# Performance work log

Measured on AMD Instinct MI355X. Metric: run time of the kernel, lower is better.

Reference implementation:

```python
import jax, jax.numpy as jnp
import numpy as np

B, T, K, H = 8, 1024, 512, 8
MASKED = True

def setup_inputs() -> dict:
    key = jax.random.key(0)
    ks = jax.random.split(key, 6)
    s = 0.02
    return {
        "x": jax.random.normal(ks[0], (B, T, K), dtype=jnp.float32),
        "Wq": jax.random.normal(ks[1], (K, H * K), dtype=jnp.float32) * s,
        "Wk": jax.random.normal(ks[2], (K, H * K), dtype=jnp.float32) * s,
        "Wv": jax.random.normal(ks[3], (K, H * K), dtype=jnp.float32) * s,
        "Wu": jax.random.normal(ks[4], (H * K, K), dtype=jnp.float32) * s,
        "bu": jnp.zeros((K,), dtype=jnp.float32),
    }

def reference(x, Wq, Wk, Wv, Wu, bu):
    b, t, k = x.shape
    h = H
    scale = k ** (-0.25)  # applied to both q and k, as in the torch module
    q = (x @ Wq).reshape(b, t, h, k) * scale
    kk = (x @ Wk).reshape(b, t, h, k) * scale
    v = (x @ Wv).reshape(b, t, h, k)
    # scores: [b, h, t_q, t_k]
    dot = jnp.einsum("bthk,bshk->bhts", q, kk)
    if MASKED:
        causal = jnp.tril(jnp.ones((t, t), dtype=bool))
        dot = jnp.where(causal, dot, -jnp.inf)
    attn = jax.nn.softmax(dot, axis=-1)
    out = jnp.einsum("bhts,bshk->bthk", attn, v).reshape(b, t, h * k)
    return out @ Wu + bu
```

## Files before the change

kernel.cpp:

```cpp
#include <hip/hip_runtime.h>
#include <hip/hip_bf16.h>

#define T_SEQ 1024
#define NH 8
#define DH 512
#define HK 4096

typedef __attribute__((ext_vector_type(8))) __bf16 bf16x8;
typedef __attribute__((ext_vector_type(4))) float f32x4;

#define QK_SCALE 0.21022410381342863f
#define QK_SCALE_LOG2E 0.30328926584f

static __device__ __forceinline__ unsigned short f2bu(float f) {
  union { __hip_bfloat16 h; unsigned short u; } cv;
  cv.h = __float2bfloat16(f);
  return cv.u;
}

#define GLOAD_LDS16(gsrc, ldst) \
  __builtin_amdgcn_global_load_lds((const __attribute__((address_space(1))) void*)(gsrc), \
                                   (__attribute__((address_space(3))) void*)(ldst), 16, 0, 0)

__global__ void cvt_bf16_kernel(const float* __restrict__ in, unsigned short* __restrict__ out, int n4) {
  int i = blockIdx.x * blockDim.x + threadIdx.x;
  if (i >= n4) return;
  const float4 v = reinterpret_cast<const float4*>(in)[i];
  ushort4 u; u.x = f2bu(v.x); u.y = f2bu(v.y); u.z = f2bu(v.z); u.w = f2bu(v.w);
  reinterpret_cast<ushort4*>(out)[i] = u;
}

__global__ void transpose_cvt_kernel(const float* __restrict__ in, unsigned short* __restrict__ out,
                                     int R, int C) {
  __shared__ float tile[32][33];
  const int c0 = blockIdx.x * 32, r0 = blockIdx.y * 32;
  const int tx = threadIdx.x, ty = threadIdx.y;
  #pragma unroll
  for (int i = ty; i < 32; i += 8)
    tile[i][tx] = in[(size_t)(r0 + i) * C + (c0 + tx)];
  __syncthreads();
  #pragma unroll
  for (int i = ty; i < 32; i += 8)
    out[(size_t)(c0 + i) * R + (r0 + tx)] = f2bu(tile[tx][i]);
}

__global__ void transpose_cvt3_kernel(const float* __restrict__ Wq, const float* __restrict__ Wk,
                                      const float* __restrict__ Wv, unsigned short* __restrict__ out) {
  __shared__ float tile[32][33];
  const float* in = (blockIdx.z == 0) ? Wq : (blockIdx.z == 1) ? Wk : Wv;
  unsigned short* dst = out + (size_t)blockIdx.z * 4096 * 512;
  const int c0 = blockIdx.x * 32, r0 = blockIdx.y * 32;
  const int tx = threadIdx.x, ty = threadIdx.y;
  #pragma unroll
  for (int i = ty; i < 32; i += 8)
    tile[i][tx] = in[(size_t)(r0 + i) * 4096 + (c0 + tx)];
  __syncthreads();
  #pragma unroll
  for (int i = ty; i < 32; i += 8)
    dst[(size_t)(c0 + i) * 512 + (r0 + tx)] = f2bu(tile[tx][i]);
}

__global__ __launch_bounds__(512, 1)
void gemm_qkv(const unsigned short* __restrict__ A,
              const unsigned short* __restrict__ B,
              unsigned short* __restrict__ Qo,
              unsigned short* __restrict__ Ko,
              unsigned short* __restrict__ Vo) {
  __shared__ __align__(16) char smem[131072];
  const int tid = threadIdx.x, lane = tid & 63, w = tid >> 6;
  const int wm = w >> 2, wn = w & 3;
  const int bid = blockIdx.x;
  const int x = bid & 7, inner = bid >> 3;
  const int p0 = (x * 6 + inner % 6) * 256;
  const int p1 = (inner / 6) * 256;

  f32x4 acc[8][4];
  #pragma unroll
  for (int i = 0; i < 8; ++i)
    #pragma unroll
    for (int j = 0; j < 4; ++j)
      acc[i][j] = f32x4{0.f, 0.f, 0.f, 0.f};

  auto stage = [&](int t, int c) {
    const int kt = t * 128;
    #pragma unroll
    for (int is = 0; is < 4; ++is) {
      const int ob = is * 8192 + w * 1024;
      const int ol = ob + lane * 16;
      const int row = ol >> 7, bo = ol & 127;
      const int sw = (row & 7) << 4;
      GLOAD_LDS16((const char*)A + (size_t)(p0 + row) * 1024 + kt + (bo ^ sw),
                  smem + c * 32768 + ob);
      GLOAD_LDS16((const char*)B + (size_t)(p1 + row) * 1024 + kt + (bo ^ sw),
                  smem + 65536 + c * 32768 + ob);
    }
  };

  stage(0, 0);
  stage(1, 1);
  asm volatile("s_waitcnt vmcnt(8)" ::: "memory");
  __builtin_amdgcn_sched_barrier(0);
  __builtin_amdgcn_s_barrier();

  for (int t = 0; t < 8; ++t) {
    const int c = t & 1;
    const char* Ab = smem + c * 32768;
    const char* Bb = smem + 65536 + c * 32768;
    #pragma unroll
    for (int ks = 0; ks < 2; ++ks) {
      bf16x8 af[8], bf[4];
      #pragma unroll
      for (int mi = 0; mi < 8; ++mi) {
        const int row = wm * 128 + mi * 16 + (lane & 15);
        af[mi] = *reinterpret_cast<const bf16x8*>(
            Ab + row * 128 + ((ks * 64 + ((lane >> 4) << 4)) ^ ((row & 7) << 4)));
      }
      #pragma unroll
      for (int ni = 0; ni < 4; ++ni) {
        const int row = wn * 64 + ni * 16 + (lane & 15);
        bf[ni] = *reinterpret_cast<const bf16x8*>(
            Bb + row * 128 + ((ks * 64 + ((lane >> 4) << 4)) ^ ((row & 7) << 4)));
      }
      #pragma unroll
      for (int mi = 0; mi < 8; ++mi)
        #pragma unroll
        for (int ni = 0; ni < 4; ++ni)
          acc[mi][ni] = __builtin_amdgcn_mfma_f32_16x16x32_bf16(af[mi], bf[ni], acc[mi][ni], 0, 0, 0);
    }
    asm volatile("" ::: "memory");
    __builtin_amdgcn_sched_barrier(0);
    __builtin_amdgcn_s_barrier();
    if (t + 2 < 8) stage(t + 2, c);
    if (t + 1 < 8) {
      if (t + 2 < 8) asm volatile("s_waitcnt vmcnt(8)" ::: "memory");
      else           asm volatile("s_waitcnt vmcnt(0)" ::: "memory");
      __builtin_amdgcn_sched_barrier(0);
      __builtin_amdgcn_s_barrier();
    }
  }

  const int region = p0 >> 12;
  if (region < 2) {
    const float qs = (region == 0) ? QK_SCALE_LOG2E : QK_SCALE;
    unsigned short* dst = (region == 0) ? Qo : Ko;
    #pragma unroll
    for (int mi = 0; mi < 8; ++mi) {
      #pragma unroll
      for (int ni = 0; ni < 4; ++ni) {
        const int n = p0 + wm * 128 + mi * 16 + ((lane >> 4) << 2);
        const int m = p1 + wn * 64 + ni * 16 + (lane & 15);
        const int b = m >> 10, t = m & 1023;
        const int nr = n & 4095, h = nr >> 9, d = nr & 511;
        ushort4 u;
        u.x = f2bu(acc[mi][ni][0] * qs); u.y = f2bu(acc[mi][ni][1] * qs);
        u.z = f2bu(acc[mi][ni][2] * qs); u.w = f2bu(acc[mi][ni][3] * qs);
        *reinterpret_cast<ushort4*>(&dst[((size_t)((b * NH + h) * T_SEQ + t)) * DH + d]) = u;
      }
    }
  } else {
    __builtin_amdgcn_sched_barrier(0);
    __builtin_amdgcn_s_barrier();
    unsigned short* Vl = reinterpret_cast<unsigned short*>(smem);
    #pragma unroll
    for (int mi = 0; mi < 8; ++mi) {
      #pragma unroll
      for (int ni = 0; ni < 4; ++ni) {
        const int dl0 = wm * 128 + mi * 16 + ((lane >> 4) << 2);
        const int tl = wn * 64 + ni * 16 + (lane & 15);
        #pragma unroll
        for (int r = 0; r < 4; ++r) {
          const int dl = dl0 + r;
          Vl[dl * 256 + (tl ^ ((dl & 7) << 3))] = f2bu(acc[mi][ni][r]);
        }
      }
    }
    __syncthreads();
    const int bb = p1 >> 10, t0 = p1 & 1023;
    const int hh = (p0 - 8192) >> 9, d0 = (p0 - 8192) & 511;
    unsigned short* vdst = Vo + ((size_t)(bb * NH + hh) * DH + d0) * T_SEQ + t0;
    #pragma unroll
    for (int i = 0; i < 16; ++i) {
      const int idx = i * 512 + tid;
      const int dr = idx >> 5, tc = (idx & 31) * 8;
      *reinterpret_cast<uint4*>(vdst + (size_t)dr * T_SEQ + tc) =
          *reinterpret_cast<const uint4*>(Vl + dr * 256 + (tc ^ ((dr & 7) << 3)));
    }
  }
}

__global__ __launch_bounds__(256, 4)
void gemm_out(const unsigned short* __restrict__ A,
              const unsigned short* __restrict__ B,
              const float* __restrict__ bias,
              float* __restrict__ C) {
  __shared__ __align__(16) char As[8192];
  __shared__ __align__(16) char Bs[16384];
  const int tid = threadIdx.x, lane = tid & 63, w = tid >> 6;
  const int bid = blockIdx.x;
  const int x = bid & 7, inner = bid >> 3;
  const int mtiles_per_xcd = gridDim.x >> 7;
  const int c0 = (inner & 15) * 32;
  const int m0 = (x * mtiles_per_xcd + (inner >> 4)) * 64;
  const int Kd = HK;

  f32x4 acc[2];
  acc[0] = f32x4{0.f, 0.f, 0.f, 0.f};
  acc[1] = f32x4{0.f, 0.f, 0.f, 0.f};

  for (int kt = 0; kt < Kd; kt += 128) {
    __syncthreads();
    #pragma unroll
    for (int is = 0; is < 2; ++is) {
      const int ob = is * 4096 + w * 1024;
      const int ol = ob + lane * 16;
      const int row = ol >> 8, bo = ol & 255;
      GLOAD_LDS16((const char*)A + ((size_t)(c0 + row) * Kd + kt) * 2 + (bo ^ ((row & 15) << 4)), As + ob);
    }
    #pragma unroll
    for (int is = 0; is < 4; ++is) {
      const int ob = is * 4096 + w * 1024;
      const int ol = ob + lane * 16;
      const int row = ol >> 8, bo = ol & 255;
      GLOAD_LDS16((const char*)B + ((size_t)(m0 + row) * Kd + kt) * 2 + (bo ^ ((row & 15) << 4)), Bs + ob);
    }
    __syncthreads();
    #pragma unroll
    for (int ks = 0; ks < 4; ++ks) {
      const int ko = ks * 64 + ((lane >> 4) << 4);
      bf16x8 af0, af1, bf;
      { const int row = (lane & 15);
        af0 = *reinterpret_cast<const bf16x8*>(As + row * 256 + (ko ^ ((row & 15) << 4))); }
      { const int row = 16 + (lane & 15);
        af1 = *reinterpret_cast<const bf16x8*>(As + row * 256 + (ko ^ ((row & 15) << 4))); }
      { const int row = w * 16 + (lane & 15);
        bf = *reinterpret_cast<const bf16x8*>(Bs + row * 256 + (ko ^ ((row & 15) << 4))); }
      acc[0] = __builtin_amdgcn_mfma_f32_16x16x32_bf16(af0, bf, acc[0], 0, 0, 0);
      acc[1] = __builtin_amdgcn_mfma_f32_16x16x32_bf16(af1, bf, acc[1], 0, 0, 0);
    }
  }

  const int m = m0 + w * 16 + (lane & 15);
  #pragma unroll
  for (int fc = 0; fc < 2; ++fc) {
    const int c = c0 + fc * 16 + ((lane >> 4) << 2);
    const float4 bn = *reinterpret_cast<const float4*>(&bias[c]);
    float4 v;
    v.x = acc[fc][0] + bn.x; v.y = acc[fc][1] + bn.y;
    v.z = acc[fc][2] + bn.z; v.w = acc[fc][3] + bn.w;
    *reinterpret_cast<float4*>(&C[(size_t)m * DH + c]) = v;
  }
}

__global__ __launch_bounds__(512, 1)
void attn_kernel(const unsigned short* __restrict__ Qg,
                 const unsigned short* __restrict__ Kg,
                 const unsigned short* __restrict__ Vtg,
                 unsigned short* __restrict__ Og) {
  __shared__ __align__(16) char Ks[2][32768];
  __shared__ __align__(16) char Vts[2][32768];
  __shared__ float S_lds[64 * 32];
  __shared__ __align__(16) char P_lds[64 * 64];
  __shared__ float Mrow[64], Lrow[64], Arow[64];
  __shared__ int rflag;

  const int tid = threadIdx.x, lane = tid & 63, w = tid >> 6;
  const int n = blockIdx.x;
  const int h = n & 7, p = (n >> 3) & 7, b = n >> 6;
  const int bh = b * NH + h;

  const unsigned short* Qbase = Qg + (size_t)bh * T_SEQ * DH;
  const char* Kbase = (const char*)(Kg + (size_t)bh * T_SEQ * DH);
  const char* Vbase = (const char*)(Vtg + (size_t)bh * DH * T_SEQ);

  auto stage = [&](int st, int buf) {
    #pragma unroll
    for (int is = 0; is < 4; ++is) {
      const int ob = is * 8192 + w * 1024;
      const int ol = ob + lane * 16;
      { const int row = ol >> 10, bo = ol & 1023;
        GLOAD_LDS16(Kbase + (size_t)(st * 32 + row) * 1024 + (bo ^ ((row & 7) << 4)), Ks[buf] + ob); }
      { const int row = ol >> 6, bo = ol & 63;
        GLOAD_LDS16(Vbase + (size_t)row * 2048 + st * 64 + (bo ^ ((row & 3) << 4)), Vts[buf] + ob); }
    }
  };

  for (int rep = 0; rep < 2; ++rep) {
    const int qt = rep ? 15 - p : p;
    const int nst = 2 * qt + 2;
    __syncthreads();

    bf16x8 qreg[16];
    {
      const int qrow = qt * 64 + ((w >> 1) << 4) + (lane & 15);
      const unsigned short* qp = Qbase + (size_t)qrow * DH + ((lane >> 4) << 3);
      #pragma unroll
      for (int k2 = 0; k2 < 16; ++k2)
        qreg[k2] = *reinterpret_cast<const bf16x8*>(qp + k2 * 32);
    }

    f32x4 o[2][8];
    #pragma unroll
    for (int mi = 0; mi < 2; ++mi)
      #pragma unroll
      for (int ni = 0; ni < 8; ++ni)
        o[mi][ni] = f32x4{0.f, 0.f, 0.f, 0.f};

    if (tid < 64) { Mrow[tid] = -INFINITY; Lrow[tid] = 0.f; }

    int cur = 0;
    stage(0, 0);

    for (int st = 0; st < nst; ++st) {
      __syncthreads();
      if (st + 1 < nst) stage(st + 1, cur ^ 1);
      if (tid == 0) rflag = 0;

      {
        const int krow = ((w & 1) << 4) + (lane & 15);
        const char* kr = Ks[cur] + krow * 1024;
        const int sw = (krow & 7) << 4;
        f32x4 sA = f32x4{0.f, 0.f, 0.f, 0.f};
        f32x4 sB = f32x4{0.f, 0.f, 0.f, 0.f};
        __builtin_amdgcn_s_setprio(1);
        #pragma unroll
        for (int ks = 0; ks < 16; ks += 2) {
          bf16x8 kf0 = *reinterpret_cast<const bf16x8*>(kr + ((ks * 64 + ((lane >> 4) << 4)) ^ sw));
          bf16x8 kf1 = *reinterpret_cast<const bf16x8*>(kr + (((ks + 1) * 64 + ((lane >> 4) << 4)) ^ sw));
          sA = __builtin_amdgcn_mfma_f32_16x16x32_bf16(qreg[ks], kf0, sA, 0, 0, 0);
          sB = __builtin_amdgcn_mfma_f32_16x16x32_bf16(qreg[ks + 1], kf1, sB, 0, 0, 0);
        }
        __builtin_amdgcn_s_setprio(0);
        const f32x4 s = sA + sB;
        const int col = ((w & 1) << 4) + (lane & 15);
        const int rbase = ((w >> 1) << 4) + ((lane >> 4) << 2);
        #pragma unroll
        for (int r = 0; r < 4; ++r)
          S_lds[(rbase + r) * 32 + (col ^ (((rbase + r) & 7) << 2))] = s[r];
      }
      asm volatile("s_waitcnt lgkmcnt(0)" ::: "memory");
      __builtin_amdgcn_sched_barrier(0);
      __builtin_amdgcn_s_barrier();

      {
        const int r = tid >> 3, cg = tid & 7;
        const int grow = qt * 64 + r;
        const int base = r * 32 + ((cg * 4) ^ ((r & 7) << 2));
        float sv[4];
        #pragma unroll
        for (int j = 0; j < 4; ++j) {
          const int c = cg * 4 + j;
          const float x = S_lds[base + j];
          sv[j] = (st * 32 + c > grow) ? -INFINITY : x;
        }
        float pm = fmaxf(fmaxf(sv[0], sv[1]), fmaxf(sv[2], sv[3]));
        pm = fmaxf(pm, __shfl_xor(pm, 1));
        pm = fmaxf(pm, __shfl_xor(pm, 2));
        pm = fmaxf(pm, __shfl_xor(pm, 4));
        const float m_old = Mrow[r];
        const bool defer = (pm <= m_old + 11.0f);
        const float m_new = defer ? m_old : pm;
        float ps;
        ushort4 pu;
        { float p0 = exp2f(sv[0] - m_new), p1 = exp2f(sv[1] - m_new),
                p2 = exp2f(sv[2] - m_new), p3 = exp2f(sv[3] - m_new);
          ps = p0 + p1 + p2 + p3;
          pu.x = f2bu(p0); pu.y = f2bu(p1); pu.z = f2bu(p2); pu.w = f2bu(p3); }
        *reinterpret_cast<ushort4*>(P_lds + r * 64 + ((cg * 8) ^ ((r & 3) << 4))) = pu;
        ps += __shfl_xor(ps, 1);
        ps += __shfl_xor(ps, 2);
        ps += __shfl_xor(ps, 4);
        if (cg == 0) {
          const float alpha = defer ? 1.0f : exp2f(m_old - m_new);
          if (!defer) { rflag = 1; Mrow[r] = m_new; }
          Arow[r] = alpha;
          Lrow[r] = alpha * Lrow[r] + ps;
        }
      }
      asm volatile("s_waitcnt lgkmcnt(0)" ::: "memory");
      __builtin_amdgcn_sched_barrier(0);
      __builtin_amdgcn_s_barrier();

      {
        bf16x8 pf[2];
        #pragma unroll
        for (int mi = 0; mi < 2; ++mi) {
          const int pr = ((w >> 2) << 5) + mi * 16 + (lane & 15);
          pf[mi] = *reinterpret_cast<const bf16x8*>(
              P_lds + pr * 64 + ((((lane >> 4) << 4)) ^ ((pr & 3) << 4)));
        }
        if (rflag) {
          #pragma unroll
          for (int mi = 0; mi < 2; ++mi) {
            const int rb = ((w >> 2) << 5) + mi * 16 + ((lane >> 4) << 2);
            const f32x4 al = f32x4{Arow[rb], Arow[rb + 1], Arow[rb + 2], Arow[rb + 3]};
            #pragma unroll
            for (int ni = 0; ni < 8; ++ni) o[mi][ni] *= al;
          }
        }
        __builtin_amdgcn_s_setprio(1);
        #pragma unroll
        for (int ni = 0; ni < 8; ++ni) {
          const int vr = ((w & 3) << 7) + ni * 16 + (lane & 15);
          bf16x8 vf = *reinterpret_cast<const bf16x8*>(
              Vts[cur] + vr * 64 + ((((lane >> 4) << 4)) ^ ((vr & 3) << 4)));
          o[0][ni] = __builtin_amdgcn_mfma_f32_16x16x32_bf16(pf[0], vf, o[0][ni], 0, 0, 0);
          o[1][ni] = __builtin_amdgcn_mfma_f32_16x16x32_bf16(pf[1], vf, o[1][ni], 0, 0, 0);
        }
        __builtin_amdgcn_s_setprio(0);
      }
      cur ^= 1;
    }

    #pragma unroll
    for (int mi = 0; mi < 2; ++mi) {
      const int rb = ((w >> 2) << 5) + mi * 16 + ((lane >> 4) << 2);
      f32x4 li;
      #pragma unroll
      for (int r = 0; r < 4; ++r) li[r] = 1.f / Lrow[rb + r];
      #pragma unroll
      for (int ni = 0; ni < 8; ++ni) {
        const int d = ((w & 3) << 7) + ni * 16 + (lane & 15);
        const size_t base = ((size_t)(b * T_SEQ + qt * 64 + rb) * NH + h) * DH + d;
        #pragma unroll
        for (int r = 0; r < 4; ++r)
          Og[base + (size_t)r * NH * DH] = f2bu(o[mi][ni][r] * li[r]);
      }
    }
  }
}

extern "C" void kernel_launch(void* const* d_in, const int* in_sizes, int n_in,
                              void* d_out, int out_size, void* d_ws, size_t ws_size,
                              hipStream_t stream) {
  (void)in_sizes; (void)n_in; (void)out_size;
  const float* x  = (const float*)d_in[0];
  const float* Wq = (const float*)d_in[1];
  const float* Wk = (const float*)d_in[2];
  const float* Wv = (const float*)d_in[3];
  const float* Wu = (const float*)d_in[4];
  const float* bu = (const float*)d_in[5];
  float* out = (float*)d_out;

  const size_t PERS = (size_t)8192 * 512 * 2 + 3 * (size_t)4096 * 512 * 2 + (size_t)512 * 4096 * 2;
  int NB = 8;
  while (NB > 1 && PERS + 4 * ((size_t)NB * 1024 * 4096 * 2) + 65536 > ws_size) NB >>= 1;

  size_t off = 0;
  auto wsp = [&](size_t bytes) {
    char* p = (char*)d_ws + off;
    off += (bytes + 255) & ~(size_t)255;
    return p;
  };
  unsigned short* xb   = (unsigned short*)wsp((size_t)8192 * 512 * 2);
  unsigned short* Wcat = (unsigned short*)wsp(3 * (size_t)4096 * 512 * 2);
  unsigned short* Wut  = (unsigned short*)wsp((size_t)512 * 4096 * 2);
  const size_t CHB = (size_t)NB * 1024 * 4096 * 2;
  unsigned short* Qc = (unsigned short*)wsp(CHB);
  unsigned short* Kc = (unsigned short*)wsp(CHB);
  unsigned short* Vc = (unsigned short*)wsp(CHB);
  unsigned short* Oc = (unsigned short*)wsp(CHB);

  cvt_bf16_kernel<<<4096, 256, 0, stream>>>(x, xb, 8192 * 512 / 4);
  transpose_cvt3_kernel<<<dim3(128, 16, 3), dim3(32, 8), 0, stream>>>(Wq, Wk, Wv, Wcat);
  transpose_cvt_kernel<<<dim3(16, 128), dim3(32, 8), 0, stream>>>(Wu, Wut, 4096, 512);

  const int nchunks = 8 / NB;
  for (int c = 0; c < nchunks; ++c) {
    const unsigned short* xc = xb + (size_t)c * NB * 1024 * 512;
    gemm_qkv<<<192 * NB, 512, 0, stream>>>(Wcat, xc, Qc, Kc, Vc);
    attn_kernel<<<64 * NB, 512, 0, stream>>>(Qc, Kc, Vc, Oc);
    gemm_out<<<256 * NB, 256, 0, stream>>>(Wut, Oc, bu, out + (size_t)c * NB * 1024 * 512);
  }
}
```

Measured before the change: 405.4 us.

## Use 64-key single-buffered tiles in attention instead of double-buffered 32-key tiles

The attention loop now processes 64 keys per step with one K/V LDS buffer, replacing 32-key double-buffered stages. This halves the number of steps and their barriers and softmax reduction rounds, and widens the softmax and PV work per step. In exchange, prefetch overlap is lost: each step loads its tile and waits at a barrier before computing, which exposes global load latency. The LDS swizzles are also reworked for the wider rows.

```diff
diff --git a/kernel.cpp b/kernel.cpp
--- a/kernel.cpp
+++ b/kernel.cpp
@@ -256,10 +256,10 @@
                  const unsigned short* __restrict__ Kg,
                  const unsigned short* __restrict__ Vtg,
                  unsigned short* __restrict__ Og) {
-  __shared__ __align__(16) char Ks[2][32768];
-  __shared__ __align__(16) char Vts[2][32768];
-  __shared__ float S_lds[64 * 32];
-  __shared__ __align__(16) char P_lds[64 * 64];
+  __shared__ __align__(16) char Ks[65536];
+  __shared__ __align__(16) char Vts[65536];
+  __shared__ float S_lds[64 * 64];
+  __shared__ __align__(16) char P_lds[64 * 128];
   __shared__ float Mrow[64], Lrow[64], Arow[64];
   __shared__ int rflag;
 
@@ -272,21 +272,20 @@
   const char* Kbase = (const char*)(Kg + (size_t)bh * T_SEQ * DH);
   const char* Vbase = (const char*)(Vtg + (size_t)bh * DH * T_SEQ);
 
-  auto stage = [&](int st, int buf) {
-    #pragma unroll
-    for (int is = 0; is < 4; ++is) {
-      const int ob = is * 8192 + w * 1024;
-      const int ol = ob + lane * 16;
-      { const int row = ol >> 10, bo = ol & 1023;
-        GLOAD_LDS16(Kbase + (size_t)(st * 32 + row) * 1024 + (bo ^ ((row & 7) << 4)), Ks[buf] + ob); }
-      { const int row = ol >> 6, bo = ol & 63;
-        GLOAD_LDS16(Vbase + (size_t)row * 2048 + st * 64 + (bo ^ ((row & 3) << 4)), Vts[buf] + ob); }
+  auto stage = [&](int st) {
+    #pragma unroll
+    for (int is = 0; is < 8; ++is) {
+      const int ob = is * 8192 + tid * 16;
+      { const int row = ob >> 10, bo = ob & 1023;
+        GLOAD_LDS16(Kbase + (size_t)(st * 64 + row) * 1024 + (bo ^ ((row & 7) << 4)), Ks + ob); }
+      { const int dr = ob >> 7, bo = ob & 127;
+        GLOAD_LDS16(Vbase + (size_t)dr * 2048 + st * 128 + (bo ^ ((dr & 7) << 4)), Vts + ob); }
     }
   };
 
   for (int rep = 0; rep < 2; ++rep) {
     const int qt = rep ? 15 - p : p;
-    const int nst = 2 * qt + 2;
+    const int nst = qt + 1;
     __syncthreads();
 
     bf16x8 qreg[16];
@@ -307,35 +306,36 @@
 
     if (tid < 64) { Mrow[tid] = -INFINITY; Lrow[tid] = 0.f; }
 
-    int cur = 0;
-    stage(0, 0);
-
     for (int st = 0; st < nst; ++st) {
       __syncthreads();
-      if (st + 1 < nst) stage(st + 1, cur ^ 1);
+      stage(st);
       if (tid == 0) rflag = 0;
+      __syncthreads();
 
       {
-        const int krow = ((w & 1) << 4) + (lane & 15);
-        const char* kr = Ks[cur] + krow * 1024;
-        const int sw = (krow & 7) << 4;
-        f32x4 sA = f32x4{0.f, 0.f, 0.f, 0.f};
-        f32x4 sB = f32x4{0.f, 0.f, 0.f, 0.f};
-        __builtin_amdgcn_s_setprio(1);
-        #pragma unroll
-        for (int ks = 0; ks < 16; ks += 2) {
-          bf16x8 kf0 = *reinterpret_cast<const bf16x8*>(kr + ((ks * 64 + ((lane >> 4) << 4)) ^ sw));
-          bf16x8 kf1 = *reinterpret_cast<const bf16x8*>(kr + (((ks + 1) * 64 + ((lane >> 4) << 4)) ^ sw));
-          sA = __builtin_amdgcn_mfma_f32_16x16x32_bf16(qreg[ks], kf0, sA, 0, 0, 0);
-          sB = __builtin_amdgcn_mfma_f32_16x16x32_bf16(qreg[ks + 1], kf1, sB, 0, 0, 0);
-        }
-        __builtin_amdgcn_s_setprio(0);
-        const f32x4 s = sA + sB;
-        const int col = ((w & 1) << 4) + (lane & 15);
-        const int rbase = ((w >> 1) << 4) + ((lane >> 4) << 2);
-        #pragma unroll
-        for (int r = 0; r < 4; ++r)
-          S_lds[(rbase + r) * 32 + (col ^ (((rbase + r) & 7) << 2))] = s[r];
+        const int rg = w >> 1;
+        #pragma unroll
+        for (int f = 0; f < 2; ++f) {
+          const int cf = (w & 1) + f * 2;
+          const int krow = cf * 16 + (lane & 15);
+          const char* kr = Ks + krow * 1024;
+          const int sw = (krow & 7) << 4;
+          f32x4 s = f32x4{0.f, 0.f, 0.f, 0.f};
+          __builtin_amdgcn_s_setprio(1);
+          #pragma unroll
+          for (int ks = 0; ks < 16; ++ks) {
+            bf16x8 kf = *reinterpret_cast<const bf16x8*>(kr + ((ks * 64 + ((lane >> 4) << 4)) ^ sw));
+            s = __builtin_amdgcn_mfma_f32_16x16x32_bf16(qreg[ks], kf, s, 0, 0, 0);
+          }
+          __builtin_amdgcn_s_setprio(0);
+          const int col = cf * 16 + (lane & 15);
+          const int rbase = rg * 16 + ((lane >> 4) << 2);
+          #pragma unroll
+          for (int r = 0; r < 4; ++r) {
+            const int row = rbase + r;
+            S_lds[row * 64 + (col ^ ((row & 7) << 3))] = s[r];
+          }
+        }
       }
       asm volatile("s_waitcnt lgkmcnt(0)" ::: "memory");
       __builtin_amdgcn_sched_barrier(0);
@@ -344,28 +344,32 @@
       {
         const int r = tid >> 3, cg = tid & 7;
         const int grow = qt * 64 + r;
-        const int base = r * 32 + ((cg * 4) ^ ((r & 7) << 2));
-        float sv[4];
-        #pragma unroll
-        for (int j = 0; j < 4; ++j) {
-          const int c = cg * 4 + j;
-          const float x = S_lds[base + j];
-          sv[j] = (st * 32 + c > grow) ? -INFINITY : x;
-        }
-        float pm = fmaxf(fmaxf(sv[0], sv[1]), fmaxf(sv[2], sv[3]));
+        const int base = r * 64 + ((cg * 8) ^ ((r & 7) << 3));
+        float sv[8];
+        #pragma unroll
+        for (int j = 0; j < 8; ++j) {
+          const int c = cg * 8 + j;
+          const float xv = S_lds[base + j];
+          sv[j] = (st * 64 + c > grow) ? -INFINITY : xv;
+        }
+        float pm = sv[0];
+        #pragma unroll
+        for (int j = 1; j < 8; ++j) pm = fmaxf(pm, sv[j]);
         pm = fmaxf(pm, __shfl_xor(pm, 1));
         pm = fmaxf(pm, __shfl_xor(pm, 2));
         pm = fmaxf(pm, __shfl_xor(pm, 4));
         const float m_old = Mrow[r];
         const bool defer = (pm <= m_old + 11.0f);
         const float m_new = defer ? m_old : pm;
-        float ps;
-        ushort4 pu;
-        { float p0 = exp2f(sv[0] - m_new), p1 = exp2f(sv[1] - m_new),
-                p2 = exp2f(sv[2] - m_new), p3 = exp2f(sv[3] - m_new);
-          ps = p0 + p1 + p2 + p3;
-          pu.x = f2bu(p0); pu.y = f2bu(p1); pu.z = f2bu(p2); pu.w = f2bu(p3); }
-        *reinterpret_cast<ushort4*>(P_lds + r * 64 + ((cg * 8) ^ ((r & 3) << 4))) = pu;
+        float ps = 0.f;
+        union { unsigned short s[8]; uint4 v; } pu;
+        #pragma unroll
+        for (int j = 0; j < 8; ++j) {
+          const float pj = exp2f(sv[j] - m_new);
+          ps += pj;
+          pu.s[j] = f2bu(pj);
+        }
+        *reinterpret_cast<uint4*>(P_lds + r * 128 + ((cg * 16) ^ ((r & 7) << 4))) = pu.v;
         ps += __shfl_xor(ps, 1);
         ps += __shfl_xor(ps, 2);
         ps += __shfl_xor(ps, 4);
@@ -381,12 +385,16 @@
       __builtin_amdgcn_s_barrier();
 
       {
-        bf16x8 pf[2];
+        bf16x8 pf[2][2];
         #pragma unroll
         for (int mi = 0; mi < 2; ++mi) {
           const int pr = ((w >> 2) << 5) + mi * 16 + (lane & 15);
-          pf[mi] = *reinterpret_cast<const bf16x8*>(
-              P_lds + pr * 64 + ((((lane >> 4) << 4)) ^ ((pr & 3) << 4)));
+          const char* prow = P_lds + pr * 128;
+          const int sw = (pr & 7) << 4;
+          #pragma unroll
+          for (int hh2 = 0; hh2 < 2; ++hh2)
+            pf[mi][hh2] = *reinterpret_cast<const bf16x8*>(
+                prow + ((hh2 * 64 + ((lane >> 4) << 4)) ^ sw));
         }
         if (rflag) {
           #pragma unroll
@@ -401,14 +409,18 @@
         #pragma unroll
         for (int ni = 0; ni < 8; ++ni) {
           const int vr = ((w & 3) << 7) + ni * 16 + (lane & 15);
-          bf16x8 vf = *reinterpret_cast<const bf16x8*>(
-              Vts[cur] + vr * 64 + ((((lane >> 4) << 4)) ^ ((vr & 3) << 4)));
-          o[0][ni] = __builtin_amdgcn_mfma_f32_16x16x32_bf16(pf[0], vf, o[0][ni], 0, 0, 0);
-          o[1][ni] = __builtin_amdgcn_mfma_f32_16x16x32_bf16(pf[1], vf, o[1][ni], 0, 0, 0);
+          const char* vrow = Vts + vr * 128;
+          const int sw = (vr & 7) << 4;
+          #pragma unroll
+          for (int hh2 = 0; hh2 < 2; ++hh2) {
+            bf16x8 vf = *reinterpret_cast<const bf16x8*>(
+                vrow + ((hh2 * 64 + ((lane >> 4) << 4)) ^ sw));
+            o[0][ni] = __builtin_amdgcn_mfma_f32_16x16x32_bf16(pf[0][hh2], vf, o[0][ni], 0, 0, 0);
+            o[1][ni] = __builtin_amdgcn_mfma_f32_16x16x32_bf16(pf[1][hh2], vf, o[1][ni], 0, 0, 0);
+          }
         }
         __builtin_amdgcn_s_setprio(0);
       }
-      cur ^= 1;
     }
 
     #pragma unroll
```

Result: slower. 480.1 us (+18.4%).
